# Kernel optimization log

Hardware: AMD Instinct MI355X
Metric: run time of the kernel (lower is better)

## Reference

```python
import jax, jax.numpy as jnp
import numpy as np


def _gat_layer(h, mask, w, a_src, a_dst):
    # h: [B,C,N,Fin], w: [C,H,Fin,Fout], a_*: [C,H,Fout,1], mask: [B,N,N] (True where no edge)
    h_prime = jnp.einsum('bcni,chio->bchno', h, w)          # [B,C,H,N,Fout]
    t = jnp.tanh(h_prime)
    s = jnp.einsum('bchno,cho->bchn', t, a_src[..., 0])      # src scores
    d = jnp.einsum('bchno,cho->bchn', t, a_dst[..., 0])      # dst scores
    attn = s[..., :, None] + d[..., None, :]                 # [B,C,H,N,N]
    attn = jnp.where(attn >= 0, attn, 0.2 * attn)            # leaky_relu(0.2)
    attn = jnp.where(mask[:, None, None, :, :], jnp.float32(-1e12), attn)
    attn = jax.nn.softmax(attn, axis=-1)
    return jnp.einsum('bchnm,bchmo->bchno', attn, h_prime)   # [B,C,H,N,Fout]


def setup_inputs() -> dict:
    key = jax.random.key(0)
    ks = jax.random.split(key, 8)
    B, C, N, F0, H, F = 2, 2, 1024, 64, 8, 64

    def xavier(k, shape):
        fan_in, fan_out = shape[-2], shape[-1]
        lim = (6.0 / (fan_in + fan_out)) ** 0.5
        return jax.random.uniform(k, shape, jnp.float32, -lim, lim)

    x = jax.random.normal(ks[0], (B, C, N, F0), dtype=jnp.float32)
    adj = jax.random.randint(ks[1], (B, N, N), 0, 2, dtype=jnp.int32)
    w1 = xavier(ks[2], (C, H, F0, F))
    a_src1 = xavier(ks[3], (C, H, F, 1))
    a_dst1 = xavier(ks[4], (C, H, F, 1))
    w2 = xavier(ks[5], (C, H, H * F, F))
    a_src2 = xavier(ks[6], (C, H, F, 1))
    a_dst2 = xavier(ks[7], (C, H, F, 1))
    return {"x": x, "adj": adj, "w1": w1, "a_src1": a_src1, "a_dst1": a_dst1,
            "w2": w2, "a_src2": a_src2, "a_dst2": a_dst2}


def reference(x, adj, w1, a_src1, a_dst1, w2, a_src2, a_dst2):
    B, C, N, _ = x.shape
    adj_f = adj.astype(jnp.float32) + jnp.eye(N, dtype=jnp.float32)[None]  # add self-loops
    mask = adj_f == 0                                        # [B,N,N]
    out1 = _gat_layer(x, mask, w1, a_src1, a_dst1)           # [B,C,H,N,F]
    # permute heads next to features, flatten, elu (dropout is identity in eval)
    x1 = jax.nn.elu(jnp.transpose(out1, (0, 1, 3, 2, 4)).reshape(B, C, N, -1))
    out2 = _gat_layer(x1, mask, w2, a_src2, a_dst2)          # [B,C,H,N,F]
    return out2.mean(axis=2)                                 # mean over heads -> [B,C,N,F]
```

## Files before the change

### kernel.cpp

```cpp
#include <hip/hip_runtime.h>
#include <hip/hip_bf16.h>

#define BB 2
#define CC 2
#define NN 1024
#define F0V 64
#define HH 8
#define FFV 64
#define BCHN (BB*CC*HH)
#define SVN  (BB*CC*HH*NN)

typedef _Float16 f16x8 __attribute__((ext_vector_type(8)));
typedef _Float16 f16x4 __attribute__((ext_vector_type(4)));
typedef __fp16 h16x2 __attribute__((ext_vector_type(2)));
typedef float f32x4 __attribute__((ext_vector_type(4)));

__global__ __launch_bounds__(256) void prep_kernel(
    const float* __restrict__ x, const int* __restrict__ adj,
    const float* __restrict__ w1, const float* __restrict__ w2,
    _Float16* __restrict__ xh, _Float16* __restrict__ w1T, _Float16* __restrict__ w2T,
    unsigned long long* __restrict__ bmg)
{
  __shared__ __align__(16) _Float16 tile[64*72];
  const int bx = blockIdx.x;
  const int t = threadIdx.x;
  if (bx < 256) {
    const int i = bx*256 + t;
    const float4 v = ((const float4*)x)[i];
    f16x4 o; o[0]=(_Float16)v.x; o[1]=(_Float16)v.y; o[2]=(_Float16)v.z; o[3]=(_Float16)v.w;
    ((f16x4*)xh)[i] = o;
  } else if (bx < 400) {
    int ch, k0, K; const float* w; _Float16* wT;
    if (bx < 272) { ch = bx - 256; k0 = 0; K = 64; w = w1; wT = w1T; }
    else { const int u = bx - 272; ch = u >> 3; k0 = (u & 7)*64; K = 512; w = w2; wT = w2T; }
    const float* src = w + ((size_t)ch*K + k0)*64;
    #pragma unroll
    for (int j = 0; j < 4; ++j) {
      const int u = t + j*256;
      const int k = u >> 4, seg = u & 15;
      const float4 v = ((const float4*)src)[(size_t)k*16 + seg];
      tile[(seg*4+0)*72 + k] = (_Float16)v.x;
      tile[(seg*4+1)*72 + k] = (_Float16)v.y;
      tile[(seg*4+2)*72 + k] = (_Float16)v.z;
      tile[(seg*4+3)*72 + k] = (_Float16)v.w;
    }
    __syncthreads();
    _Float16* dst = wT + (size_t)ch*64*K + k0;
    #pragma unroll
    for (int j = 0; j < 2; ++j) {
      const int u = t + j*256;
      const int f = u >> 3, seg = u & 7;
      const f16x8 o = *(const f16x8*)&tile[f*72 + seg*8];
      *(f16x8*)(dst + (size_t)f*K + seg*8) = o;
    }
  } else {
    const int wg = (bx - 400)*4 + (t >> 6);
    const int lane = t & 63;
    for (int idx = wg; idx < BB*NN*16; idx += 1024) {
      const int b = idx >> 14;
      const int n = (idx >> 4) & (NN - 1);
      const int word = idx & 15;
      const int m = word*64 + lane;
      const int pred = (adj[((size_t)b*NN + n)*NN + m] != 0) || (m == n);
      unsigned long long bits = __ballot(pred);
      if (lane == 0) bmg[idx] = bits;
    }
  }
}

template<int K>
__global__ __launch_bounds__(256) void proj_mfma(
    const _Float16* __restrict__ A,
    const _Float16* __restrict__ wT,
    const float* __restrict__ asrc, const float* __restrict__ adst,
    _Float16* __restrict__ HpT, float* __restrict__ s_out, float* __restrict__ d_out)
{
  __shared__ float sp[4][32], sd[4][32];
  const int bch = blockIdx.y;
  const int h = bch % HH; const int bc = bch / HH; const int c = bc % CC;
  const int row0 = blockIdx.x*32;
  const int t = threadIdx.x;
  const int w = t >> 6, lane = t & 63;
  const int colr = lane & 15, quad = lane >> 4;

  const _Float16* Arow0 = A + ((size_t)bc*NN + row0 + colr)*K;
  const _Float16* Arow1 = Arow0 + (size_t)16*K;
  const _Float16* Brow  = wT + ((size_t)(c*HH + h)*64 + w*16 + colr)*K;

  f32x4 acc0 = {0.f,0.f,0.f,0.f}, acc1 = {0.f,0.f,0.f,0.f};
  #pragma unroll 4
  for (int kb = 0; kb < K; kb += 32) {
    const f16x8 a0 = *(const f16x8*)(Arow0 + kb + quad*8);
    const f16x8 a1 = *(const f16x8*)(Arow1 + kb + quad*8);
    const f16x8 bf = *(const f16x8*)(Brow  + kb + quad*8);
    acc0 = __builtin_amdgcn_mfma_f32_16x16x32_f16(a0, bf, acc0, 0, 0, 0);
    acc1 = __builtin_amdgcn_mfma_f32_16x16x32_f16(a1, bf, acc1, 0, 0, 0);
  }

  const float af = asrc[(c*HH + h)*64 + w*16 + colr];
  const float bf_ = adst[(c*HH + h)*64 + w*16 + colr];
  _Float16* HT = HpT + ((size_t)bch*64 + w*16 + colr)*NN + row0;

  #pragma unroll
  for (int mt = 0; mt < 2; ++mt) {
    const f32x4 a = mt ? acc1 : acc0;
    f16x4 hv;
    #pragma unroll
    for (int i = 0; i < 4; ++i) {
      const float v = a[i];
      hv[i] = (_Float16)v;
      const float ex = __expf(2.f*v);
      const float th = 1.f - 2.f/(ex + 1.f);
      float ps = th * af, pd = th * bf_;
      #pragma unroll
      for (int off = 1; off < 16; off <<= 1) {
        ps += __shfl_xor(ps, off);
        pd += __shfl_xor(pd, off);
      }
      if (colr == 0) {
        sp[w][mt*16 + quad*4 + i] = ps;
        sd[w][mt*16 + quad*4 + i] = pd;
      }
    }
    *(f16x4*)(HT + mt*16 + quad*4) = hv;
  }
  __syncthreads();
  if (t < 32) {
    const float sv = sp[0][t] + sp[1][t] + sp[2][t] + sp[3][t];
    const float dv = sd[0][t] + sd[1][t] + sd[2][t] + sd[3][t];
    s_out[bch*NN + row0 + t] = sv;
    d_out[bch*NN + row0 + t] = dv;
  }
}

template<int LAYER>
__global__ __launch_bounds__(256, 4) void attn_mfma(
    const _Float16* __restrict__ HpT, const float* __restrict__ s_arr,
    const float* __restrict__ d_arr, const unsigned long long* __restrict__ bmg,
    _Float16* __restrict__ outp)
{
  __shared__ float partials[4][32*68];
  __shared__ float dsP[4][32];
  const int bch = blockIdx.x;
  const int b = bch / (CC*HH);
  const int row0 = blockIdx.y*32;
  const int t = threadIdx.x;
  const int w = t >> 6, lane = t & 63;
  const int colr = lane & 15, quad = lane >> 4;

  const float* dg = d_arr + (size_t)bch*NN;
  const float4* dg4 = (const float4*)dg;
  float mxl = -1e30f;
  #pragma unroll
  for (int j = 0; j < 4; ++j) {
    const float4 v = dg4[lane + 64*j];
    mxl = fmaxf(fmaxf(v.x, v.y), fmaxf(fmaxf(v.z, v.w), mxl));
  }
  #pragma unroll
  for (int off = 1; off < 64; off <<= 1) mxl = fmaxf(mxl, __shfl_xor(mxl, off));
  const float maxd = mxl;

  const int r0 = row0 + colr, r1 = r0 + 16;
  const float s0 = s_arr[(size_t)bch*NN + r0];
  const float s1 = s_arr[(size_t)bch*NN + r1];
  const float so0 = s0 + maxd, so1 = s1 + maxd;
  const float offs0 = fmaxf(so0, 0.2f*so0);
  const float offs1 = fmaxf(so1, 0.2f*so1);
  const float sA0 = s0 - offs0, sB0 = 0.2f*s0 - offs0;
  const float sA1 = s1 - offs1, sB1 = 0.2f*s1 - offs1;

  unsigned long long m0[4], m1[4];
  {
    const unsigned long long* bm0 = bmg + ((size_t)b*NN + r0)*16 + w*4;
    const unsigned long long* bm1 = bmg + ((size_t)b*NN + r1)*16 + w*4;
    #pragma unroll
    for (int j = 0; j < 4; ++j) { m0[j] = bm0[j]; m1[j] = bm1[j]; }
  }

  const _Float16* Bg = HpT + (size_t)bch*64*NN;
  const int kbase = w*256;
  const _Float16* Bp = Bg + kbase + quad*8;

  f32x4 acc[2][4], accs[2];
  #pragma unroll
  for (int rt = 0; rt < 2; ++rt) {
    accs[rt] = (f32x4){0.f,0.f,0.f,0.f};
    #pragma unroll
    for (int ft = 0; ft < 4; ++ft) acc[rt][ft] = (f32x4){0.f,0.f,0.f,0.f};
  }
  f16x8 ones;
  #pragma unroll
  for (int i = 0; i < 8; ++i) ones[i] = (_Float16)1.f;

  f16x8 Bc[4];
  #pragma unroll
  for (int ft = 0; ft < 4; ++ft) Bc[ft] = *(const f16x8*)(Bp + (size_t)(ft*16 + colr)*NN);
  float4 dc0 = *(const float4*)(dg + kbase + quad*8);
  float4 dc1 = *(const float4*)(dg + kbase + quad*8 + 4);

  #pragma unroll
  for (int ks = 0; ks < 8; ++ks) {
    f16x8 Bn[4]; float4 dn0, dn1;
    if (ks < 7) {
      #pragma unroll
      for (int ft = 0; ft < 4; ++ft)
        Bn[ft] = *(const f16x8*)(Bp + (size_t)(ft*16 + colr)*NN + (ks+1)*32);
      dn0 = *(const float4*)(dg + kbase + (ks+1)*32 + quad*8);
      dn1 = *(const float4*)(dg + kbase + (ks+1)*32 + quad*8 + 4);
    }
    const unsigned mb0 = (unsigned)((m0[ks >> 1] >> ((ks & 1)*32 + quad*8)) & 0xFFull);
    const unsigned mb1 = (unsigned)((m1[ks >> 1] >> ((ks & 1)*32 + quad*8)) & 0xFFull);
    const float dd[8] = {dc0.x, dc0.y, dc0.z, dc0.w, dc1.x, dc1.y, dc1.z, dc1.w};
    union { f16x8 v; h16x2 h[4]; } A0, A1;
    #pragma unroll
    for (int jp = 0; jp < 4; ++jp) {
      float p0[2], p1[2];
      #pragma unroll
      for (int jj = 0; jj < 2; ++jj) {
        const int j = jp*2 + jj;
        const float dj = dd[j];
        const float l0 = fmaxf(sA0 + dj, fmaf(0.2f, dj, sB0));
        const float l1 = fmaxf(sA1 + dj, fmaf(0.2f, dj, sB1));
        p0[jj] = ((mb0 >> j) & 1u) ? __expf(l0) : 0.f;
        p1[jj] = ((mb1 >> j) & 1u) ? __expf(l1) : 0.f;
      }
      A0.h[jp] = __builtin_amdgcn_cvt_pkrtz(p0[0], p0[1]);
      A1.h[jp] = __builtin_amdgcn_cvt_pkrtz(p1[0], p1[1]);
    }
    #pragma unroll
    for (int ft = 0; ft < 4; ++ft) {
      acc[0][ft] = __builtin_amdgcn_mfma_f32_16x16x32_f16(A0.v, Bc[ft], acc[0][ft], 0, 0, 0);
      acc[1][ft] = __builtin_amdgcn_mfma_f32_16x16x32_f16(A1.v, Bc[ft], acc[1][ft], 0, 0, 0);
    }
    accs[0] = __builtin_amdgcn_mfma_f32_16x16x32_f16(A0.v, ones, accs[0], 0, 0, 0);
    accs[1] = __builtin_amdgcn_mfma_f32_16x16x32_f16(A1.v, ones, accs[1], 0, 0, 0);
    if (ks < 7) {
      #pragma unroll
      for (int ft = 0; ft < 4; ++ft) Bc[ft] = Bn[ft];
      dc0 = dn0; dc1 = dn1;
    }
  }

  if (colr == 0) {
    #pragma unroll
    for (int i = 0; i < 4; ++i) {
      dsP[w][quad*4 + i] = accs[0][i];
      dsP[w][16 + quad*4 + i] = accs[1][i];
    }
  }
  float* pw = partials[w];
  #pragma unroll
  for (int rt = 0; rt < 2; ++rt)
    #pragma unroll
    for (int ft = 0; ft < 4; ++ft)
      #pragma unroll
      for (int i = 0; i < 4; ++i)
        pw[(rt*16 + quad*4 + i)*68 + ft*16 + colr] = acc[rt][ft][i];
  __syncthreads();

  const int r = t >> 3, f0 = (t & 7)*8;
  const float dsum = dsP[0][r] + dsP[1][r] + dsP[2][r] + dsP[3][r];
  const float inv = 1.f / dsum;
  float4 c0 = {0.f,0.f,0.f,0.f}, c1 = {0.f,0.f,0.f,0.f};
  #pragma unroll
  for (int w4 = 0; w4 < 4; ++w4) {
    const float* base = &partials[w4][r*68 + f0];
    const float4 a0 = *(const float4*)base;
    const float4 a1 = *(const float4*)(base + 4);
    c0.x += a0.x; c0.y += a0.y; c0.z += a0.z; c0.w += a0.w;
    c1.x += a1.x; c1.y += a1.y; c1.z += a1.z; c1.w += a1.w;
  }
  const float cv[8] = {c0.x,c0.y,c0.z,c0.w, c1.x,c1.y,c1.z,c1.w};
  f16x8 o;
  #pragma unroll
  for (int i = 0; i < 8; ++i) {
    float v = cv[i] * inv;
    if (LAYER == 1) v = v > 0.f ? v : expm1f(v);
    o[i] = (_Float16)v;
  }
  const int bc = bch / HH, h = bch % HH;
  if (LAYER == 1)
    *(f16x8*)(outp + ((size_t)bc*NN + row0 + r)*512 + h*64 + f0) = o;
  else
    *(f16x8*)(outp + ((size_t)bch*NN + row0 + r)*64 + f0) = o;
}

__global__ __launch_bounds__(256) void reduce_heads(
    const _Float16* __restrict__ out2, float* __restrict__ out)
{
  const int o = blockIdx.x*256 + threadIdx.x;
  const int f = o & 63;
  const int n = (o >> 6) & (NN - 1);
  const int bc = o >> 16;
  float acc = 0.f;
  #pragma unroll
  for (int h = 0; h < HH; ++h)
    acc += (float)out2[(((size_t)bc*HH + h)*NN + n)*FFV + f];
  out[o] = acc * 0.125f;
}

extern "C" void kernel_launch(void* const* d_in, const int* in_sizes, int n_in,
                              void* d_out, int out_size, void* d_ws, size_t ws_size,
                              hipStream_t stream)
{
  const float* x   = (const float*)d_in[0];
  const int*   adj = (const int*)d_in[1];
  const float* w1  = (const float*)d_in[2];
  const float* as1 = (const float*)d_in[3];
  const float* ad1 = (const float*)d_in[4];
  const float* w2  = (const float*)d_in[5];
  const float* as2 = (const float*)d_in[6];
  const float* ad2 = (const float*)d_in[7];

  char* w8 = (char*)d_ws;
  _Float16* HpT = (_Float16*)(w8);
  _Float16* XB  = (_Float16*)(w8 + (4u<<20));
  _Float16* xh  = (_Float16*)(w8 + (8u<<20));
  _Float16* w1T = (_Float16*)(w8 + (8u<<20) + (512u<<10));
  _Float16* w2T = (_Float16*)(w8 + (8u<<20) + (768u<<10));
  float* s_v = (float*)(w8 + (10u<<20));
  float* d_v = (float*)(w8 + (10u<<20) + SVN*4);
  unsigned long long* bmg = (unsigned long long*)(w8 + (10u<<20) + SVN*8);

  prep_kernel<<<656, 256, 0, stream>>>(x, adj, w1, w2, xh, w1T, w2T, bmg);
  proj_mfma<64><<<dim3(NN/32, BCHN), 256, 0, stream>>>(xh, w1T, as1, ad1, HpT, s_v, d_v);
  attn_mfma<1><<<dim3(BCHN, NN/32), 256, 0, stream>>>(HpT, s_v, d_v, bmg, XB);
  proj_mfma<512><<<dim3(NN/32, BCHN), 256, 0, stream>>>(XB, w2T, as2, ad2, HpT, s_v, d_v);
  attn_mfma<2><<<dim3(BCHN, NN/32), 256, 0, stream>>>(HpT, s_v, d_v, bmg, XB);
  reduce_heads<<<dim3((unsigned)(out_size/256)), 256, 0, stream>>>(XB, (float*)d_out);
}
```

Measured before the change: 164.2 us.

## Fuse all GAT stages into one persistent kernel with grid barriers

```diff
diff --git a/kernel.cpp b/kernel.cpp
--- a/kernel.cpp
+++ b/kernel.cpp
@@ -1,48 +1,73 @@
 #include <hip/hip_runtime.h>
-#include <hip/hip_bf16.h>
 
 #define BB 2
 #define CC 2
 #define NN 1024
-#define F0V 64
 #define HH 8
-#define FFV 64
-#define BCHN (BB*CC*HH)
-#define SVN  (BB*CC*HH*NN)
+#define BCHN 32
+#define SVN (BCHN*NN)
+#define NBLK 512
+#define LOG2E 1.44269504f
 
 typedef _Float16 f16x8 __attribute__((ext_vector_type(8)));
 typedef _Float16 f16x4 __attribute__((ext_vector_type(4)));
 typedef __fp16 h16x2 __attribute__((ext_vector_type(2)));
 typedef float f32x4 __attribute__((ext_vector_type(4)));
 
-__global__ __launch_bounds__(256) void prep_kernel(
+union SmemU {
+  _Float16 tile[64*72];
+  struct { float sp[4][32]; float sd[4][32]; } pr;
+  struct { float partials[4][32*68]; float dsP[4][32]; } at;
+};
+
+__device__ __forceinline__ float fexp2(float x) {
+  float r; asm("v_exp_f32 %0, %1" : "=v"(r) : "v"(x)); return r;
+}
+
+__device__ __forceinline__ void gbar(unsigned* cnt, unsigned* gen, unsigned g) {
+  __syncthreads();
+  if (threadIdx.x == 0) {
+    __threadfence();
+    if (atomicAdd(cnt, 1u) == g*(unsigned)NBLK - 1u) atomicAdd(gen, 1u);
+    int guard = 0;
+    while (__hip_atomic_load(gen, __ATOMIC_RELAXED, __HIP_MEMORY_SCOPE_AGENT) < g) {
+      __builtin_amdgcn_s_sleep(8);
+      if (++guard > (1 << 20)) break;
+    }
+    __threadfence();
+  }
+  __syncthreads();
+}
+
+__device__ __forceinline__ void prep_phase(
     const float* __restrict__ x, const int* __restrict__ adj,
     const float* __restrict__ w1, const float* __restrict__ w2,
     _Float16* __restrict__ xh, _Float16* __restrict__ w1T, _Float16* __restrict__ w2T,
-    unsigned long long* __restrict__ bmg)
-{
-  __shared__ __align__(16) _Float16 tile[64*72];
-  const int bx = blockIdx.x;
-  const int t = threadIdx.x;
-  if (bx < 256) {
-    const int i = bx*256 + t;
-    const float4 v = ((const float4*)x)[i];
-    f16x4 o; o[0]=(_Float16)v.x; o[1]=(_Float16)v.y; o[2]=(_Float16)v.z; o[3]=(_Float16)v.w;
-    ((f16x4*)xh)[i] = o;
-  } else if (bx < 400) {
+    unsigned long long* __restrict__ bmg, SmemU& sm)
+{
+  const int b = blockIdx.x, t = threadIdx.x;
+  if (b < 128) {
+    #pragma unroll
+    for (int j = 0; j < 2; ++j) {
+      const int i = b*512 + j*256 + t;
+      const float4 v = ((const float4*)x)[i];
+      f16x4 o; o[0]=(_Float16)v.x; o[1]=(_Float16)v.y; o[2]=(_Float16)v.z; o[3]=(_Float16)v.w;
+      ((f16x4*)xh)[i] = o;
+    }
+  } else if (b < 272) {
     int ch, k0, K; const float* w; _Float16* wT;
-    if (bx < 272) { ch = bx - 256; k0 = 0; K = 64; w = w1; wT = w1T; }
-    else { const int u = bx - 272; ch = u >> 3; k0 = (u & 7)*64; K = 512; w = w2; wT = w2T; }
+    if (b < 144) { ch = b - 128; k0 = 0; K = 64; w = w1; wT = w1T; }
+    else { const int u = b - 144; ch = u >> 3; k0 = (u & 7)*64; K = 512; w = w2; wT = w2T; }
     const float* src = w + ((size_t)ch*K + k0)*64;
     #pragma unroll
     for (int j = 0; j < 4; ++j) {
       const int u = t + j*256;
       const int k = u >> 4, seg = u & 15;
       const float4 v = ((const float4*)src)[(size_t)k*16 + seg];
-      tile[(seg*4+0)*72 + k] = (_Float16)v.x;
-      tile[(seg*4+1)*72 + k] = (_Float16)v.y;
-      tile[(seg*4+2)*72 + k] = (_Float16)v.z;
-      tile[(seg*4+3)*72 + k] = (_Float16)v.w;
+      sm.tile[(seg*4+0)*72 + k] = (_Float16)v.x;
+      sm.tile[(seg*4+1)*72 + k] = (_Float16)v.y;
+      sm.tile[(seg*4+2)*72 + k] = (_Float16)v.z;
+      sm.tile[(seg*4+3)*72 + k] = (_Float16)v.w;
     }
     __syncthreads();
     _Float16* dst = wT + (size_t)ch*64*K + k0;
@@ -50,18 +75,18 @@
     for (int j = 0; j < 2; ++j) {
       const int u = t + j*256;
       const int f = u >> 3, seg = u & 7;
-      const f16x8 o = *(const f16x8*)&tile[f*72 + seg*8];
+      const f16x8 o = *(const f16x8*)&sm.tile[f*72 + seg*8];
       *(f16x8*)(dst + (size_t)f*K + seg*8) = o;
     }
   } else {
-    const int wg = (bx - 400)*4 + (t >> 6);
+    const int wg = (b - 272)*4 + (t >> 6);
     const int lane = t & 63;
-    for (int idx = wg; idx < BB*NN*16; idx += 1024) {
-      const int b = idx >> 14;
+    for (int idx = wg; idx < BB*NN*16; idx += 960) {
+      const int bb = idx >> 14;
       const int n = (idx >> 4) & (NN - 1);
       const int word = idx & 15;
       const int m = word*64 + lane;
-      const int pred = (adj[((size_t)b*NN + n)*NN + m] != 0) || (m == n);
+      const int pred = (adj[((size_t)bb*NN + n)*NN + m] != 0) || (m == n);
       unsigned long long bits = __ballot(pred);
       if (lane == 0) bmg[idx] = bits;
     }
@@ -69,16 +94,15 @@
 }
 
 template<int K>
-__global__ __launch_bounds__(256) void proj_mfma(
-    const _Float16* __restrict__ A,
-    const _Float16* __restrict__ wT,
+__device__ __forceinline__ void proj_unit(
+    int u, const _Float16* __restrict__ A, const _Float16* __restrict__ wT,
     const float* __restrict__ asrc, const float* __restrict__ adst,
-    _Float16* __restrict__ HpT, float* __restrict__ s_out, float* __restrict__ d_out)
-{
-  __shared__ float sp[4][32], sd[4][32];
-  const int bch = blockIdx.y;
-  const int h = bch % HH; const int bc = bch / HH; const int c = bc % CC;
-  const int row0 = blockIdx.x*32;
+    _Float16* __restrict__ HpT, float* __restrict__ s_out, float* __restrict__ d_out,
+    SmemU& sm)
+{
+  const int bch = u & 31;
+  const int row0 = (u >> 5) * 32;
+  const int h = bch & 7; const int bc = bch >> 3; const int c = bc & 1;
   const int t = threadIdx.x;
   const int w = t >> 6, lane = t & 63;
   const int colr = lane & 15, quad = lane >> 4;
@@ -97,7 +121,7 @@
     acc1 = __builtin_amdgcn_mfma_f32_16x16x32_f16(a1, bf, acc1, 0, 0, 0);
   }
 
-  const float af = asrc[(c*HH + h)*64 + w*16 + colr];
+  const float af  = asrc[(c*HH + h)*64 + w*16 + colr];
   const float bf_ = adst[(c*HH + h)*64 + w*16 + colr];
   _Float16* HT = HpT + ((size_t)bch*64 + w*16 + colr)*NN + row0;
 
@@ -118,32 +142,32 @@
         pd += __shfl_xor(pd, off);
       }
       if (colr == 0) {
-        sp[w][mt*16 + quad*4 + i] = ps;
-        sd[w][mt*16 + quad*4 + i] = pd;
+        sm.pr.sp[w][mt*16 + quad*4 + i] = ps;
+        sm.pr.sd[w][mt*16 + quad*4 + i] = pd;
       }
     }
     *(f16x4*)(HT + mt*16 + quad*4) = hv;
   }
   __syncthreads();
   if (t < 32) {
-    const float sv = sp[0][t] + sp[1][t] + sp[2][t] + sp[3][t];
-    const float dv = sd[0][t] + sd[1][t] + sd[2][t] + sd[3][t];
-    s_out[bch*NN + row0 + t] = sv;
-    d_out[bch*NN + row0 + t] = dv;
-  }
+    const float sv = sm.pr.sp[0][t] + sm.pr.sp[1][t] + sm.pr.sp[2][t] + sm.pr.sp[3][t];
+    const float dv = sm.pr.sd[0][t] + sm.pr.sd[1][t] + sm.pr.sd[2][t] + sm.pr.sd[3][t];
+    s_out[bch*NN + row0 + t] = sv * LOG2E;
+    d_out[bch*NN + row0 + t] = dv * LOG2E;
+  }
+  __syncthreads();
 }
 
 template<int LAYER>
-__global__ __launch_bounds__(256, 4) void attn_mfma(
+__device__ __forceinline__ void attn_unit(
     const _Float16* __restrict__ HpT, const float* __restrict__ s_arr,
     const float* __restrict__ d_arr, const unsigned long long* __restrict__ bmg,
-    _Float16* __restrict__ outp)
-{
-  __shared__ float partials[4][32*68];
-  __shared__ float dsP[4][32];
-  const int bch = blockIdx.x;
-  const int b = bch / (CC*HH);
-  const int row0 = blockIdx.y*32;
+    _Float16* __restrict__ outp, SmemU& sm)
+{
+  const int bidx = blockIdx.x;
+  const int bch = bidx & 31;
+  const int row0 = (bidx >> 5) * 32;
+  const int bb = bch >> 4;
   const int t = threadIdx.x;
   const int w = t >> 6, lane = t & 63;
   const int colr = lane & 15, quad = lane >> 4;
@@ -160,30 +184,25 @@
   for (int off = 1; off < 64; off <<= 1) mxl = fmaxf(mxl, __shfl_xor(mxl, off));
   const float maxd = mxl;
 
-  const int r0 = row0 + colr, r1 = r0 + 16;
-  const float s0 = s_arr[(size_t)bch*NN + r0];
-  const float s1 = s_arr[(size_t)bch*NN + r1];
-  const float so0 = s0 + maxd, so1 = s1 + maxd;
-  const float offs0 = fmaxf(so0, 0.2f*so0);
-  const float offs1 = fmaxf(so1, 0.2f*so1);
-  const float sA0 = s0 - offs0, sB0 = 0.2f*s0 - offs0;
-  const float sA1 = s1 - offs1, sB1 = 0.2f*s1 - offs1;
-
-  unsigned long long m0[4], m1[4];
-  {
-    const unsigned long long* bm0 = bmg + ((size_t)b*NN + r0)*16 + w*4;
-    const unsigned long long* bm1 = bmg + ((size_t)b*NN + r1)*16 + w*4;
-    #pragma unroll
-    for (int j = 0; j < 4; ++j) { m0[j] = bm0[j]; m1[j] = bm1[j]; }
-  }
-
-  const _Float16* Bg = HpT + (size_t)bch*64*NN;
-  const int kbase = w*256;
-  const _Float16* Bp = Bg + kbase + quad*8;
-
-  f32x4 acc[2][4], accs[2];
-  #pragma unroll
-  for (int rt = 0; rt < 2; ++rt) {
+  float sA[4], sB[4];
+  const unsigned long long* bmp[4];
+  #pragma unroll
+  for (int rt = 0; rt < 4; ++rt) {
+    const int r = row0 + (rt >> 1)*512 + (rt & 1)*16 + colr;
+    const float s = s_arr[(size_t)bch*NN + r];
+    const float so = s + maxd;
+    const float offs = fmaxf(so, 0.2f*so);
+    sA[rt] = s - offs;
+    sB[rt] = 0.2f*s - offs;
+    bmp[rt] = bmg + ((size_t)bb*NN + r)*16 + w*4;
+  }
+
+  const _Float16* Bp = HpT + (size_t)bch*64*NN + w*256 + quad*8;
+  const float* dgk = dg + w*256 + quad*8;
+
+  f32x4 acc[4][4], accs[4];
+  #pragma unroll
+  for (int rt = 0; rt < 4; ++rt) {
     accs[rt] = (f32x4){0.f,0.f,0.f,0.f};
     #pragma unroll
     for (int ft = 0; ft < 4; ++ft) acc[rt][ft] = (f32x4){0.f,0.f,0.f,0.f};
@@ -195,8 +214,11 @@
   f16x8 Bc[4];
   #pragma unroll
   for (int ft = 0; ft < 4; ++ft) Bc[ft] = *(const f16x8*)(Bp + (size_t)(ft*16 + colr)*NN);
-  float4 dc0 = *(const float4*)(dg + kbase + quad*8);
-  float4 dc1 = *(const float4*)(dg + kbase + quad*8 + 4);
+  float4 dc0 = *(const float4*)(dgk);
+  float4 dc1 = *(const float4*)(dgk + 4);
+  unsigned long long mwc[4], mwn[4];
+  #pragma unroll
+  for (int rt = 0; rt < 4; ++rt) mwc[rt] = bmp[rt][0];
 
   #pragma unroll
   for (int ks = 0; ks < 8; ++ks) {
@@ -205,98 +227,140 @@
       #pragma unroll
       for (int ft = 0; ft < 4; ++ft)
         Bn[ft] = *(const f16x8*)(Bp + (size_t)(ft*16 + colr)*NN + (ks+1)*32);
-      dn0 = *(const float4*)(dg + kbase + (ks+1)*32 + quad*8);
-      dn1 = *(const float4*)(dg + kbase + (ks+1)*32 + quad*8 + 4);
-    }
-    const unsigned mb0 = (unsigned)((m0[ks >> 1] >> ((ks & 1)*32 + quad*8)) & 0xFFull);
-    const unsigned mb1 = (unsigned)((m1[ks >> 1] >> ((ks & 1)*32 + quad*8)) & 0xFFull);
+      dn0 = *(const float4*)(dgk + (ks+1)*32);
+      dn1 = *(const float4*)(dgk + (ks+1)*32 + 4);
+    }
+    if ((ks & 1) == 0 && ks < 6) {
+      #pragma unroll
+      for (int rt = 0; rt < 4; ++rt) mwn[rt] = bmp[rt][ks/2 + 1];
+    }
     const float dd[8] = {dc0.x, dc0.y, dc0.z, dc0.w, dc1.x, dc1.y, dc1.z, dc1.w};
-    union { f16x8 v; h16x2 h[4]; } A0, A1;
-    #pragma unroll
-    for (int jp = 0; jp < 4; ++jp) {
-      float p0[2], p1[2];
-      #pragma unroll
-      for (int jj = 0; jj < 2; ++jj) {
-        const int j = jp*2 + jj;
-        const float dj = dd[j];
-        const float l0 = fmaxf(sA0 + dj, fmaf(0.2f, dj, sB0));
-        const float l1 = fmaxf(sA1 + dj, fmaf(0.2f, dj, sB1));
-        p0[jj] = ((mb0 >> j) & 1u) ? __expf(l0) : 0.f;
-        p1[jj] = ((mb1 >> j) & 1u) ? __expf(l1) : 0.f;
+    union { f16x8 v; h16x2 h[4]; } Af[4];
+    #pragma unroll
+    for (int rt = 0; rt < 4; ++rt) {
+      const unsigned mb = (unsigned)((mwc[rt] >> ((ks & 1)*32 + quad*8)) & 0xFFull);
+      #pragma unroll
+      for (int jp = 0; jp < 4; ++jp) {
+        float pv[2];
+        #pragma unroll
+        for (int jj = 0; jj < 2; ++jj) {
+          const int j = jp*2 + jj;
+          const float dj = dd[j];
+          const float l = fmaxf(sA[rt] + dj, fmaf(0.2f, dj, sB[rt]));
+          pv[jj] = ((mb >> j) & 1u) ? fexp2(l) : 0.f;
+        }
+        Af[rt].h[jp] = __builtin_amdgcn_cvt_pkrtz(pv[0], pv[1]);
       }
-      A0.h[jp] = __builtin_amdgcn_cvt_pkrtz(p0[0], p0[1]);
-      A1.h[jp] = __builtin_amdgcn_cvt_pkrtz(p1[0], p1[1]);
-    }
-    #pragma unroll
-    for (int ft = 0; ft < 4; ++ft) {
-      acc[0][ft] = __builtin_amdgcn_mfma_f32_16x16x32_f16(A0.v, Bc[ft], acc[0][ft], 0, 0, 0);
-      acc[1][ft] = __builtin_amdgcn_mfma_f32_16x16x32_f16(A1.v, Bc[ft], acc[1][ft], 0, 0, 0);
-    }
-    accs[0] = __builtin_amdgcn_mfma_f32_16x16x32_f16(A0.v, ones, accs[0], 0, 0, 0);
-    accs[1] = __builtin_amdgcn_mfma_f32_16x16x32_f16(A1.v, ones, accs[1], 0, 0, 0);
+    }
+    #pragma unroll
+    for (int rt = 0; rt < 4; ++rt) {
+      #pragma unroll
+      for (int ft = 0; ft < 4; ++ft)
+        acc[rt][ft] = __builtin_amdgcn_mfma_f32_16x16x32_f16(Af[rt].v, Bc[ft], acc[rt][ft], 0, 0, 0);
+      accs[rt] = __builtin_amdgcn_mfma_f32_16x16x32_f16(Af[rt].v, ones, accs[rt], 0, 0, 0);
+    }
     if (ks < 7) {
       #pragma unroll
       for (int ft = 0; ft < 4; ++ft) Bc[ft] = Bn[ft];
       dc0 = dn0; dc1 = dn1;
     }
-  }
-
-  if (colr == 0) {
-    #pragma unroll
-    for (int i = 0; i < 4; ++i) {
-      dsP[w][quad*4 + i] = accs[0][i];
-      dsP[w][16 + quad*4 + i] = accs[1][i];
-    }
-  }
-  float* pw = partials[w];
-  #pragma unroll
-  for (int rt = 0; rt < 2; ++rt)
-    #pragma unroll
-    for (int ft = 0; ft < 4; ++ft)
-      #pragma unroll
-      for (int i = 0; i < 4; ++i)
-        pw[(rt*16 + quad*4 + i)*68 + ft*16 + colr] = acc[rt][ft][i];
-  __syncthreads();
-
-  const int r = t >> 3, f0 = (t & 7)*8;
-  const float dsum = dsP[0][r] + dsP[1][r] + dsP[2][r] + dsP[3][r];
-  const float inv = 1.f / dsum;
-  float4 c0 = {0.f,0.f,0.f,0.f}, c1 = {0.f,0.f,0.f,0.f};
-  #pragma unroll
-  for (int w4 = 0; w4 < 4; ++w4) {
-    const float* base = &partials[w4][r*68 + f0];
-    const float4 a0 = *(const float4*)base;
-    const float4 a1 = *(const float4*)(base + 4);
-    c0.x += a0.x; c0.y += a0.y; c0.z += a0.z; c0.w += a0.w;
-    c1.x += a1.x; c1.y += a1.y; c1.z += a1.z; c1.w += a1.w;
-  }
-  const float cv[8] = {c0.x,c0.y,c0.z,c0.w, c1.x,c1.y,c1.z,c1.w};
-  f16x8 o;
-  #pragma unroll
-  for (int i = 0; i < 8; ++i) {
-    float v = cv[i] * inv;
-    if (LAYER == 1) v = v > 0.f ? v : expm1f(v);
-    o[i] = (_Float16)v;
-  }
-  const int bc = bch / HH, h = bch % HH;
-  if (LAYER == 1)
-    *(f16x8*)(outp + ((size_t)bc*NN + row0 + r)*512 + h*64 + f0) = o;
-  else
-    *(f16x8*)(outp + ((size_t)bch*NN + row0 + r)*64 + f0) = o;
-}
-
-__global__ __launch_bounds__(256) void reduce_heads(
-    const _Float16* __restrict__ out2, float* __restrict__ out)
-{
-  const int o = blockIdx.x*256 + threadIdx.x;
-  const int f = o & 63;
-  const int n = (o >> 6) & (NN - 1);
-  const int bc = o >> 16;
-  float acc = 0.f;
-  #pragma unroll
-  for (int h = 0; h < HH; ++h)
-    acc += (float)out2[(((size_t)bc*HH + h)*NN + n)*FFV + f];
-  out[o] = acc * 0.125f;
+    if ((ks & 1) && ks < 7) {
+      #pragma unroll
+      for (int rt = 0; rt < 4; ++rt) mwc[rt] = mwn[rt];
+    }
+  }
+
+  #pragma unroll
+  for (int half = 0; half < 2; ++half) {
+    if (half) __syncthreads();
+    if (colr == 0) {
+      #pragma unroll
+      for (int rt2 = 0; rt2 < 2; ++rt2)
+        #pragma unroll
+        for (int i = 0; i < 4; ++i)
+          sm.at.dsP[w][rt2*16 + quad*4 + i] = accs[half*2 + rt2][i];
+    }
+    float* pw = sm.at.partials[w];
+    #pragma unroll
+    for (int rt2 = 0; rt2 < 2; ++rt2)
+      #pragma unroll
+      for (int ft = 0; ft < 4; ++ft)
+        #pragma unroll
+        for (int i = 0; i < 4; ++i)
+          pw[(rt2*16 + quad*4 + i)*68 + ft*16 + colr] = acc[half*2 + rt2][ft][i];
+    __syncthreads();
+
+    const int r = t >> 3, f0 = (t & 7)*8;
+    const float dsum = sm.at.dsP[0][r] + sm.at.dsP[1][r] + sm.at.dsP[2][r] + sm.at.dsP[3][r];
+    const float inv = 1.f / dsum;
+    float4 c0 = {0.f,0.f,0.f,0.f}, c1 = {0.f,0.f,0.f,0.f};
+    #pragma unroll
+    for (int w4 = 0; w4 < 4; ++w4) {
+      const float* base = &sm.at.partials[w4][r*68 + f0];
+      const float4 a0 = *(const float4*)base;
+      const float4 a1 = *(const float4*)(base + 4);
+      c0.x += a0.x; c0.y += a0.y; c0.z += a0.z; c0.w += a0.w;
+      c1.x += a1.x; c1.y += a1.y; c1.z += a1.z; c1.w += a1.w;
+    }
+    const float cv[8] = {c0.x,c0.y,c0.z,c0.w, c1.x,c1.y,c1.z,c1.w};
+    f16x8 o;
+    #pragma unroll
+    for (int i = 0; i < 8; ++i) {
+      float v = cv[i] * inv;
+      if (LAYER == 1) v = v > 0.f ? v : expm1f(v);
+      o[i] = (_Float16)v;
+    }
+    const int rfull = half*32 + r;
+    const int tile = rfull >> 4;
+    const int grow = row0 + (tile >> 1)*512 + (tile & 1)*16 + (rfull & 15);
+    const int bc = bch >> 3, h = bch & 7;
+    if (LAYER == 1)
+      *(f16x8*)(outp + ((size_t)bc*NN + grow)*512 + h*64 + f0) = o;
+    else
+      *(f16x8*)(outp + ((size_t)bch*NN + grow)*64 + f0) = o;
+  }
+}
+
+__global__ __launch_bounds__(256, 2) void gat_mega(
+    const float* __restrict__ x, const int* __restrict__ adj,
+    const float* __restrict__ w1, const float* __restrict__ as1, const float* __restrict__ ad1,
+    const float* __restrict__ w2, const float* __restrict__ as2, const float* __restrict__ ad2,
+    _Float16* __restrict__ xh, _Float16* __restrict__ w1T, _Float16* __restrict__ w2T,
+    unsigned long long* __restrict__ bmg, _Float16* __restrict__ HpT, _Float16* __restrict__ XB,
+    float* __restrict__ s_v, float* __restrict__ d_v, float* __restrict__ out,
+    unsigned* cnt, unsigned* gen)
+{
+  __shared__ SmemU sm;
+
+  prep_phase(x, adj, w1, w2, xh, w1T, w2T, bmg, sm);
+  gbar(cnt, gen, 1u);
+
+  proj_unit<64>(blockIdx.x,        xh, w1T, as1, ad1, HpT, s_v, d_v, sm);
+  proj_unit<64>(blockIdx.x + NBLK, xh, w1T, as1, ad1, HpT, s_v, d_v, sm);
+  gbar(cnt, gen, 2u);
+
+  attn_unit<1>(HpT, s_v, d_v, bmg, XB, sm);
+  gbar(cnt, gen, 3u);
+
+  proj_unit<512>(blockIdx.x,        XB, w2T, as2, ad2, HpT, s_v, d_v, sm);
+  proj_unit<512>(blockIdx.x + NBLK, XB, w2T, as2, ad2, HpT, s_v, d_v, sm);
+  gbar(cnt, gen, 4u);
+
+  attn_unit<2>(HpT, s_v, d_v, bmg, XB, sm);
+  gbar(cnt, gen, 5u);
+
+  #pragma unroll
+  for (int j = 0; j < 2; ++j) {
+    const int o = (blockIdx.x + j*NBLK)*256 + threadIdx.x;
+    const int f = o & 63;
+    const int n = (o >> 6) & (NN - 1);
+    const int bc = o >> 16;
+    float acc = 0.f;
+    #pragma unroll
+    for (int h = 0; h < HH; ++h)
+      acc += (float)XB[(((size_t)bc*HH + h)*NN + n)*64 + f];
+    out[o] = acc * 0.125f;
+  }
 }
 
 extern "C" void kernel_launch(void* const* d_in, const int* in_sizes, int n_in,
@@ -321,11 +385,10 @@
   float* s_v = (float*)(w8 + (10u<<20));
   float* d_v = (float*)(w8 + (10u<<20) + SVN*4);
   unsigned long long* bmg = (unsigned long long*)(w8 + (10u<<20) + SVN*8);
-
-  prep_kernel<<<656, 256, 0, stream>>>(x, adj, w1, w2, xh, w1T, w2T, bmg);
-  proj_mfma<64><<<dim3(NN/32, BCHN), 256, 0, stream>>>(xh, w1T, as1, ad1, HpT, s_v, d_v);
-  attn_mfma<1><<<dim3(BCHN, NN/32), 256, 0, stream>>>(HpT, s_v, d_v, bmg, XB);
-  proj_mfma<512><<<dim3(NN/32, BCHN), 256, 0, stream>>>(XB, w2T, as2, ad2, HpT, s_v, d_v);
-  attn_mfma<2><<<dim3(BCHN, NN/32), 256, 0, stream>>>(HpT, s_v, d_v, bmg, XB);
-  reduce_heads<<<dim3((unsigned)(out_size/256)), 256, 0, stream>>>(XB, (float*)d_out);
-}
+  unsigned* bar = (unsigned*)(w8 + (10u<<20) + SVN*8 + (256u<<10));
+
+  hipMemsetAsync(bar, 0, 16, stream);
+  gat_mega<<<NBLK, 256, 0, stream>>>(x, adj, w1, as1, ad1, w2, as2, ad2,
+                                     xh, w1T, w2T, bmg, HpT, XB, s_v, d_v,
+                                     (float*)d_out, bar, bar + 1);
+}
```

Result: slower. 373.3 us (+127.4%).
